# Performance work log

Measured on AMD Instinct MI355X. Metric: run time of the kernel, lower is better.

The kernel has to match this reference:

```python
import jax, jax.numpy as jnp
import numpy as np
from jax import lax

EPS = 1e-5


def setup_inputs() -> dict:
    key = jax.random.key(0)
    ks = jax.random.split(key, 8)
    b, c_in, h, w = 16, 256, 64, 64
    c_out, kh, n_exp = 512, 3, 8
    fan_in = c_in * kh * kh
    bound_w = float(np.sqrt(6.0 / fan_in))  # kaiming_uniform a=sqrt(5) -> U(-sqrt(6/fan_in), +)
    bound_b = float(1.0 / np.sqrt(fan_in))
    return {
        "x": jax.random.normal(ks[0], (b, c_in, h, w), dtype=jnp.float32),
        "expert_weight": jax.random.uniform(ks[1], (n_exp, c_out, c_in, kh, kh), jnp.float32, -bound_w, bound_w),
        "expert_bias": jax.random.uniform(ks[2], (n_exp, c_out), jnp.float32, -bound_b, bound_b),
        "fc_w": jax.random.uniform(ks[3], (n_exp, c_in), jnp.float32, -1.0 / np.sqrt(c_in), 1.0 / np.sqrt(c_in)),
        "fc_b": jax.random.uniform(ks[4], (n_exp,), jnp.float32, -1.0 / np.sqrt(c_in), 1.0 / np.sqrt(c_in)),
        "bn_gamma": jnp.ones((c_out,), jnp.float32),
        "bn_beta": jnp.zeros((c_out,), jnp.float32),
    }


def reference(x, expert_weight, expert_bias, fc_w, fc_b, bn_gamma, bn_beta):
    # --- route_func: GAP -> Linear -> sigmoid -> (b, k) ---
    pooled = x.mean(axis=(2, 3))                       # (b, c_in)
    routing = jax.nn.sigmoid(pooled @ fc_w.T + fc_b)   # (b, k)

    # --- per-sample combined kernels and biases ---
    comb_w = jnp.einsum('bk,koihw->boihw', routing, expert_weight)  # (b, c_out, c_in, kh, kw)
    comb_b = routing @ expert_bias                                  # (b, c_out)

    # --- per-sample conv (equivalent of groups=b grouped conv) ---
    def conv_one(xi, wi):
        # xi: (c_in, h, w), wi: (c_out, c_in, kh, kw)
        return lax.conv_general_dilated(
            xi[None], wi, window_strides=(1, 1), padding=[(1, 1), (1, 1)],
            rhs_dilation=(1, 1), dimension_numbers=('NCHW', 'OIHW', 'NCHW'))[0]

    out = jax.vmap(conv_one)(x, comb_w) + comb_b[:, :, None, None]  # (b, c_out, h, w)

    # --- BatchNorm2d (training mode: batch statistics) ---
    mean = out.mean(axis=(0, 2, 3))
    var = out.var(axis=(0, 2, 3))
    out = (out - mean[None, :, None, None]) * (bn_gamma * lax.rsqrt(var + EPS))[None, :, None, None] \
          + bn_beta[None, :, None, None]

    # --- LeakyReLU(0.1) ---
    return jnp.where(out > 0, out, 0.1 * out)
```

## Files before the change

### kernel.cpp

```cpp
#include <hip/hip_runtime.h>
#include <hip/hip_bf16.h>
#include <stdint.h>

typedef unsigned short u16;
typedef short bf16x8 __attribute__((ext_vector_type(8)));
typedef float f32x4 __attribute__((ext_vector_type(4)));
typedef u16 u16x8 __attribute__((ext_vector_type(8)));

#define DEVFN static __device__ __forceinline__

#define NB 16
#define CIN 256
#define HH 64
#define WW 64
#define COUT 512
#define NEXP 8
#define NPX 4096
#define KTOT 2304
#define NSTEP 72

DEVFN u16 bf16_rne(float f){
  union { float f; uint32_t u; } v; v.f = f;
  uint32_t u = v.u;
  return (u16)((u + 0x7fffu + ((u >> 16) & 1u)) >> 16);
}

DEVFN void gload16(const void* g, void* l){
  __builtin_amdgcn_global_load_lds((const __attribute__((address_space(1))) void*)g,
                                   (__attribute__((address_space(3))) void*)l,
                                   16, 0, 0);
}

__global__ void k_pool(const float* __restrict__ x, float* __restrict__ pooled){
  int bc = blockIdx.x;
  const float4* p4 = (const float4*)(x + (size_t)bc * NPX);
  int t = threadIdx.x;
  float s = 0.f;
  for (int i = t; i < NPX/4; i += 256){ float4 v = p4[i]; s += v.x+v.y+v.z+v.w; }
  for (int o = 32; o; o >>= 1) s += __shfl_down(s, o);
  __shared__ float ls[4];
  if ((t & 63) == 0) ls[t >> 6] = s;
  __syncthreads();
  if (t == 0) pooled[bc] = (ls[0]+ls[1]+ls[2]+ls[3]) * (1.0f/ (float)NPX);
}

__global__ void k_route(const float* __restrict__ pooled, const float* __restrict__ fcw,
                        const float* __restrict__ fcb, float* __restrict__ routing){
  int bk = blockIdx.x;
  int b = bk >> 3, k = bk & 7;
  int l = threadIdx.x;
  float4 pv = ((const float4*)(pooled + b*CIN))[l];
  float4 wv = ((const float4*)(fcw   + k*CIN))[l];
  float s = pv.x*wv.x + pv.y*wv.y + pv.z*wv.z + pv.w*wv.w;
  for (int o = 32; o; o >>= 1) s += __shfl_down(s, o);
  if (l == 0) routing[b*8 + k] = 1.0f / (1.0f + __expf(-(s + fcb[k])));
}

__global__ void k_cbias(const float* __restrict__ routing, const float* __restrict__ eb,
                        float* __restrict__ cbias){
  int idx = blockIdx.x*256 + threadIdx.x;
  int b = idx >> 9, co = idx & 511;
  float s = 0.f;
  for (int k = 0; k < 8; k++) s += routing[b*8+k] * eb[k*COUT + co];
  cbias[idx] = s;
}

__global__ void k_wcomb(const float* __restrict__ routing, const float* __restrict__ ew,
                        u16* __restrict__ wc){
  int blk  = blockIdx.x;
  int step = blk >> 6;
  int cog  = blk & 63;
  int cb = step / 9, rs = step - cb*9;
  int t = threadIdx.x;
  int ci = t & 31, co = cog*8 + (t >> 5);
  int cig = cb*32 + ci;
  float wv[8];
#pragma unroll
  for (int k = 0; k < 8; k++)
    wv[k] = ew[(size_t)((k*COUT + co)*CIN + cig)*9 + rs];
  for (int b = 0; b < NB; b++){
    float s = 0.f;
#pragma unroll
    for (int k = 0; k < 8; k++) s += routing[b*8+k] * wv[k];
    wc[((size_t)(b*NSTEP + step)*COUT + co)*32 + ci] = bf16_rne(s);
  }
}

__global__ void k_xprep(const float* __restrict__ x, u16* __restrict__ xt){
  int blk = blockIdx.x;
  int ctile = blk & 3;
  int h = (blk >> 2) & 63;
  int b = blk >> 8;
  __shared__ u16 S[64][66];
  int t = threadIdx.x;
  {
    int ci_l = t >> 2, w0 = (t & 3) * 16;
    const float4* src = (const float4*)(x + ((size_t)((b*CIN + ctile*64 + ci_l)*HH + h)*WW + w0));
    float4 a = src[0], bb = src[1], c = src[2], d = src[3];
    u16* row = &S[ci_l][w0];
    row[0]=bf16_rne(a.x);  row[1]=bf16_rne(a.y);  row[2]=bf16_rne(a.z);  row[3]=bf16_rne(a.w);
    row[4]=bf16_rne(bb.x); row[5]=bf16_rne(bb.y); row[6]=bf16_rne(bb.z); row[7]=bf16_rne(bb.w);
    row[8]=bf16_rne(c.x);  row[9]=bf16_rne(c.y);  row[10]=bf16_rne(c.z); row[11]=bf16_rne(c.w);
    row[12]=bf16_rne(d.x); row[13]=bf16_rne(d.y); row[14]=bf16_rne(d.z); row[15]=bf16_rne(d.w);
  }
  __syncthreads();
  {
    int w_l = t >> 2, cig = (t & 3) * 16;
    u16x8 v0, v1;
#pragma unroll
    for (int j = 0; j < 8; j++){ v0[j] = S[cig+j][w_l]; v1[j] = S[cig+8+j][w_l]; }
    u16* dst = xt + ((size_t)(b*66 + h + 1)*68 + (w_l + 1))*CIN + ctile*64 + cig;
    *(u16x8*)(dst)     = v0;
    *(u16x8*)(dst + 8) = v1;
  }
}

#define XBYTES 17408
#define WBYTES 8192

__global__ __launch_bounds__(256, 2) void k_conv(
    const u16* __restrict__ xt, const u16* __restrict__ wc,
    const float* __restrict__ cbias, float* __restrict__ out,
    float* __restrict__ ssum, float* __restrict__ ssq)
{
  __shared__ char lds[2*XBYTES + 2*WBYTES];
  char* Xb0 = lds;
  char* Xb1 = lds + XBYTES;
  char* Wb0 = lds + 2*XBYTES;
  char* Wb1 = lds + 2*XBYTES + WBYTES;

  int hw = blockIdx.x;
  int lb = (hw & 7) * 256 + (hw >> 3);
  int b  = lb >> 7;
  int ct = (lb >> 5) & 3;
  int pt = lb & 31;
  int h0 = pt * 2;

  int t = threadIdx.x, l = t & 63, wv = t >> 6;
  int wm = wv >> 1, wn = wv & 1;
  int l15 = l & 15, kbq = l >> 4;

  const u16* xtb = xt + (size_t)b * 66*68*CIN;
  const u16* wcb = wc + (size_t)(b*NSTEP) * COUT*32 + ct*128*32;


  f32x4 acc[4][4];
#pragma unroll
  for (int m = 0; m < 4; m++)
#pragma unroll
    for (int n = 0; n < 4; n++) acc[m][n] = (f32x4){0.f,0.f,0.f,0.f};

  const int byteA0 = (wm*64 + l15)*64 + ((kbq ^ ((l15 >> 1) & 3)) << 4);

  {
#pragma unroll
    for (int i = 0; i < 5; i++){
      int qb = i*256 + wv*64;
      if (qb < 1088){
        int q = qb + l;
        int t2 = q >> 2;
        int lr = (t2 * 964) >> 16;
        int c  = t2 - lr*68;
        int j  = q & 3;
        const u16* src = xtb + ((size_t)(h0 + lr)*68 + c)*CIN + 0*32 + ((j ^ ((c >> 1) & 3)) << 3);
        gload16(src, Xb0 + qb*16);
      }
    }
#pragma unroll
    for (int i = 0; i < 2; i++){
      int q = i*256 + wv*64 + l;
      int co_l = q >> 2, j = q & 3;
      const u16* src = wcb + co_l*32 + ((j ^ ((co_l >> 1) & 3)) << 3);
      gload16(src, Wb0 + (i*256 + wv*64)*16);
    }
  }
  __syncthreads();

  int step = 0;
  for (int cb = 0; cb < 8; cb++){
    char* Xc = (cb & 1) ? Xb1 : Xb0;
    char* Xn = (cb & 1) ? Xb0 : Xb1;
#pragma unroll
    for (int rs = 0; rs < 9; rs++, step++){
      const int r = rs / 3, s = rs - r*3;
      if (step < NSTEP-1){
        char* Wn = ((step+1) & 1) ? Wb1 : Wb0;
        const u16* wstep = wcb + (size_t)(step+1)*COUT*32;
#pragma unroll
        for (int i = 0; i < 2; i++){
          int q = i*256 + wv*64 + l;
          int co_l = q >> 2, j = q & 3;
          gload16(wstep + co_l*32 + ((j ^ ((co_l >> 1) & 3)) << 3),
                  Wn + (i*256 + wv*64)*16);
        }
      }
      if (rs == 8 && cb < 7){
#pragma unroll
        for (int i = 0; i < 5; i++){
          int qb = i*256 + wv*64;
          if (qb < 1088){
            int q = qb + l;
            int t2 = q >> 2;
            int lr = (t2 * 964) >> 16;
            int c  = t2 - lr*68;
            int j  = q & 3;
            const u16* src = xtb + ((size_t)(h0 + lr)*68 + c)*CIN + (cb+1)*32 + ((j ^ ((c >> 1) & 3)) << 3);
            gload16(src, Xn + qb*16);
          }
        }
      }

      char* Wc = (step & 1) ? Wb1 : Wb0;
      int c0 = l15 + s;
      int byteB0 = ((wn + r)*68 + c0)*64 + ((kbq ^ ((c0 >> 1) & 3)) << 4);

      bf16x8 af[4], bfr[4];
#pragma unroll
      for (int m = 0; m < 4; m++) af[m]  = *(const bf16x8*)(Wc + byteA0 + m*1024);
#pragma unroll
      for (int n = 0; n < 4; n++) bfr[n] = *(const bf16x8*)(Xc + byteB0 + n*1024);
#pragma unroll
      for (int m = 0; m < 4; m++)
#pragma unroll
        for (int n = 0; n < 4; n++)
          acc[m][n] = __builtin_amdgcn_mfma_f32_16x16x32_bf16(af[m], bfr[n], acc[m][n], 0, 0, 0);

      __syncthreads();
    }
  }

  int co_t = ct*128 + wm*64 + (kbq << 2);
  int px_t = pt*128 + wn*64 + l15;
  float* outb = out + (size_t)b * COUT * NPX;
#pragma unroll
  for (int m = 0; m < 4; m++){
#pragma unroll
    for (int rg = 0; rg < 4; rg++){
      int co = co_t + m*16 + rg;
      float bias = cbias[b*COUT + co];
      float s1 = 0.f, s2 = 0.f;
      size_t base = (size_t)co * NPX + px_t;
#pragma unroll
      for (int n = 0; n < 4; n++){
        float v = acc[m][n][rg] + bias;
        outb[base + n*16] = v;
        s1 += v; s2 += v*v;
      }
#pragma unroll
      for (int o = 8; o; o >>= 1){ s1 += __shfl_xor(s1, o); s2 += __shfl_xor(s2, o); }
      if (l15 == 0){ atomicAdd(&ssum[co], s1); atomicAdd(&ssq[co], s2); }
    }
  }
}

__global__ void k_stats(const float* __restrict__ ssum, const float* __restrict__ ssq,
                        const float* __restrict__ gamma, const float* __restrict__ beta,
                        float* __restrict__ sc, float* __restrict__ sh){
  int co = blockIdx.x*256 + threadIdx.x;
  const float invN = 1.0f / 65536.0f;
  float m  = ssum[co] * invN;
  float var = ssq[co] * invN - m*m;
  float scale = gamma[co] * rsqrtf(var + 1e-5f);
  sc[co] = scale;
  sh[co] = beta[co] - m*scale;
}

__global__ void k_norm(float* __restrict__ out, const float* __restrict__ sc,
                       const float* __restrict__ sh){
  const int NF4 = (NB*COUT*NPX)/4;
  int idx = blockIdx.x*256 + threadIdx.x;
  float4* o4 = (float4*)out;
  for (int i = idx; i < NF4; i += 8192*256){
    float4 v = o4[i];
    int co = (i >> 10) & 511;
    float a = sc[co], d = sh[co];
    v.x = fmaf(v.x, a, d); v.y = fmaf(v.y, a, d);
    v.z = fmaf(v.z, a, d); v.w = fmaf(v.w, a, d);
    v.x = v.x > 0.f ? v.x : 0.1f*v.x;
    v.y = v.y > 0.f ? v.y : 0.1f*v.y;
    v.z = v.z > 0.f ? v.z : 0.1f*v.z;
    v.w = v.w > 0.f ? v.w : 0.1f*v.w;
    o4[i] = v;
  }
}

extern "C" void kernel_launch(void* const* d_in, const int* in_sizes, int n_in,
                              void* d_out, int out_size, void* d_ws, size_t ws_size,
                              hipStream_t stream) {
  const float* x     = (const float*)d_in[0];
  const float* ew    = (const float*)d_in[1];
  const float* eb    = (const float*)d_in[2];
  const float* fcw   = (const float*)d_in[3];
  const float* fcb   = (const float*)d_in[4];
  const float* gamma = (const float*)d_in[5];
  const float* beta  = (const float*)d_in[6];
  float* out = (float*)d_out;

  char* ws = (char*)d_ws;
  const size_t XT_BYTES = (size_t)NB*66*68*CIN*2;
  const size_t WC_BYTES = (size_t)NB*NSTEP*COUT*32*2;
  u16* xt = (u16*)ws;
  u16* wc = (u16*)(ws + XT_BYTES);
  float* fbase   = (float*)(ws + XT_BYTES + WC_BYTES);
  float* pooled  = fbase;
  float* routing = fbase + 4096;
  float* cbias   = fbase + 4096 + 128;
  float* ssum    = cbias + 8192;
  float* ssq     = ssum + 512;
  float* sc      = ssq + 512;
  float* sh      = sc + 512;

  hipMemsetAsync(xt, 0, XT_BYTES, stream);
  hipMemsetAsync(ssum, 0, 2*512*sizeof(float), stream);

  k_pool <<<4096, 256, 0, stream>>>(x, pooled);
  k_xprep<<<4096, 256, 0, stream>>>(x, xt);
  k_route<<<128,   64, 0, stream>>>(pooled, fcw, fcb, routing);
  k_cbias<<<32,   256, 0, stream>>>(routing, eb, cbias);
  k_wcomb<<<4608, 256, 0, stream>>>(routing, ew, wc);
  k_conv <<<2048, 256, 0, stream>>>(xt, wc, cbias, out, ssum, ssq);
  k_stats<<<2,    256, 0, stream>>>(ssum, ssq, gamma, beta, sc, sh);
  k_norm <<<8192, 256, 0, stream>>>(out, sc, sh);
}
```

Measured before the change: 331.6 us.

## Triple-buffer weight tiles and issue prefetch earlier with explicit vmcnt waits

The conv main loop moves from a double-buffered weight tile to a triple buffer, so each weight tile is prefetched two steps ahead. The next input-channel X tile is now issued earlier, at step 5 instead of step 8. Manual s_waitcnt vmcnt counts plus raw s_barrier with sched_barrier replace __syncthreads, so outstanding global-to-LDS loads need not fully drain at every step. MFMA blocks are wrapped in s_setprio to favour the math waves. This raises LDS use by one weight buffer, which may affect occupancy, and depends on the hand-counted vmcnt values being correct. The X staging also issues redundant duplicate loads in place of the guarded tail.

Result: no change. 337.9 us (+1.9%).

```diff
diff --git a/kernel.cpp b/kernel.cpp
--- a/kernel.cpp
+++ b/kernel.cpp
@@ -16,7 +16,6 @@
 #define COUT 512
 #define NEXP 8
 #define NPX 4096
-#define KTOT 2304
 #define NSTEP 72
 
 DEVFN u16 bf16_rne(float f){
@@ -30,6 +29,11 @@
                                    (__attribute__((address_space(3))) void*)l,
                                    16, 0, 0);
 }
+
+#define VMWAIT(N) asm volatile("s_waitcnt vmcnt(" #N ")" ::: "memory")
+#define BARRIER() do { __builtin_amdgcn_s_barrier(); \
+                       __builtin_amdgcn_sched_barrier(0); \
+                       asm volatile("" ::: "memory"); } while(0)
 
 __global__ void k_pool(const float* __restrict__ x, float* __restrict__ pooled){
   int bc = blockIdx.x;
@@ -118,16 +122,91 @@
 #define XBYTES 17408
 #define WBYTES 8192
 
+DEVFN void stage_w(const u16* __restrict__ wstep, char* dst, int wv, int l){
+#pragma unroll
+  for (int i = 0; i < 2; i++){
+    int q = i*256 + wv*64 + l;
+    int co_l = q >> 2, j = q & 3;
+    gload16(wstep + co_l*32 + ((j ^ ((co_l >> 1) & 3)) << 3), dst + (i*256 + wv*64)*16);
+  }
+  __builtin_amdgcn_sched_barrier(0);
+}
+
+DEVFN void stage_x(const u16* __restrict__ xtb, int h0, int cioff, char* dst, int wv, int l){
+#pragma unroll
+  for (int i = 0; i < 5; i++){
+    int qb = i*256 + wv*64;
+    if (qb >= 1088) qb -= 1088;
+    int q = qb + l;
+    int t2 = q >> 2;
+    int lr = (t2 * 964) >> 16;
+    int c  = t2 - lr*68;
+    int j  = q & 3;
+    gload16(xtb + ((size_t)(h0 + lr)*68 + c)*CIN + cioff + ((j ^ ((c >> 1) & 3)) << 3),
+            dst + qb*16);
+  }
+  __builtin_amdgcn_sched_barrier(0);
+}
+
+template<int RS>
+DEVFN void conv_step(int cb, char* w0, char* w1, char* w2,
+                     const char* Xc, char* Xn,
+                     const u16* __restrict__ xtb, const u16* __restrict__ wcb, int h0,
+                     int wv, int l, int wn, int l15, int kbq, int byteA0,
+                     f32x4 acc[4][4])
+{
+  constexpr int r = RS / 3, s = RS - r*3;
+  char* Wc = (RS % 3 == 0) ? w0 : (RS % 3 == 1) ? w1 : w2;
+  char* Wp = ((RS+2) % 3 == 0) ? w0 : ((RS+2) % 3 == 1) ? w1 : w2;
+
+  int c0 = l15 + s;
+  int byteB0 = ((wn + r)*68 + c0)*64 + ((kbq ^ ((c0 >> 1) & 3)) << 4);
+  bf16x8 af[4], bfr[4];
+#pragma unroll
+  for (int m = 0; m < 4; m++) af[m]  = *(const bf16x8*)(Wc + byteA0 + m*1024);
+#pragma unroll
+  for (int n = 0; n < 4; n++) bfr[n] = *(const bf16x8*)(Xc + byteB0 + n*1024);
+
+  if constexpr (RS < 7) {
+    stage_w(wcb + (size_t)(cb*9 + RS + 2)*(COUT*32), Wp, wv, l);
+  } else {
+    if (cb != 7) stage_w(wcb + (size_t)(cb*9 + RS + 2)*(COUT*32), Wp, wv, l);
+  }
+  if constexpr (RS == 5) {
+    if (cb != 7) stage_x(xtb, h0, (cb+1)*32, Xn, wv, l);
+  }
+
+  __builtin_amdgcn_s_setprio(1);
+#pragma unroll
+  for (int m = 0; m < 4; m++)
+#pragma unroll
+    for (int n = 0; n < 4; n++)
+      acc[m][n] = __builtin_amdgcn_mfma_f32_16x16x32_bf16(af[m], bfr[n], acc[m][n], 0, 0, 0);
+  __builtin_amdgcn_s_setprio(0);
+
+  if constexpr (RS <= 4)      { VMWAIT(2); BARRIER(); }
+  else if constexpr (RS == 5 || RS == 6) {
+    if (cb != 7) { VMWAIT(7); } else { VMWAIT(2); }
+    BARRIER();
+  }
+  else if constexpr (RS == 7) {
+    if (cb != 7) { VMWAIT(2); } else { VMWAIT(0); }
+    BARRIER();
+  }
+  else                        { if (cb != 7) { VMWAIT(2); BARRIER(); } }
+}
+
 __global__ __launch_bounds__(256, 2) void k_conv(
     const u16* __restrict__ xt, const u16* __restrict__ wc,
     const float* __restrict__ cbias, float* __restrict__ out,
     float* __restrict__ ssum, float* __restrict__ ssq)
 {
-  __shared__ char lds[2*XBYTES + 2*WBYTES];
-  char* Xb0 = lds;
-  char* Xb1 = lds + XBYTES;
-  char* Wb0 = lds + 2*XBYTES;
-  char* Wb1 = lds + 2*XBYTES + WBYTES;
+  __shared__ char lds[3*WBYTES + 2*XBYTES];
+  char* w0  = lds;
+  char* w1  = lds + WBYTES;
+  char* w2  = lds + 2*WBYTES;
+  char* Xb0 = lds + 3*WBYTES;
+  char* Xb1 = lds + 3*WBYTES + XBYTES;
 
   int hw = blockIdx.x;
   int lb = (hw & 7) * 256 + (hw >> 3);
@@ -143,7 +222,6 @@
   const u16* xtb = xt + (size_t)b * 66*68*CIN;
   const u16* wcb = wc + (size_t)(b*NSTEP) * COUT*32 + ct*128*32;
 
-
   f32x4 acc[4][4];
 #pragma unroll
   for (int m = 0; m < 4; m++)
@@ -152,81 +230,24 @@
 
   const int byteA0 = (wm*64 + l15)*64 + ((kbq ^ ((l15 >> 1) & 3)) << 4);
 
-  {
-#pragma unroll
-    for (int i = 0; i < 5; i++){
-      int qb = i*256 + wv*64;
-      if (qb < 1088){
-        int q = qb + l;
-        int t2 = q >> 2;
-        int lr = (t2 * 964) >> 16;
-        int c  = t2 - lr*68;
-        int j  = q & 3;
-        const u16* src = xtb + ((size_t)(h0 + lr)*68 + c)*CIN + 0*32 + ((j ^ ((c >> 1) & 3)) << 3);
-        gload16(src, Xb0 + qb*16);
-      }
-    }
-#pragma unroll
-    for (int i = 0; i < 2; i++){
-      int q = i*256 + wv*64 + l;
-      int co_l = q >> 2, j = q & 3;
-      const u16* src = wcb + co_l*32 + ((j ^ ((co_l >> 1) & 3)) << 3);
-      gload16(src, Wb0 + (i*256 + wv*64)*16);
-    }
-  }
-  __syncthreads();
-
-  int step = 0;
+  stage_x(xtb, h0, 0, Xb0, wv, l);
+  stage_w(wcb, w0, wv, l);
+  stage_w(wcb + COUT*32, w1, wv, l);
+  VMWAIT(2);
+  BARRIER();
+
   for (int cb = 0; cb < 8; cb++){
     char* Xc = (cb & 1) ? Xb1 : Xb0;
     char* Xn = (cb & 1) ? Xb0 : Xb1;
-#pragma unroll
-    for (int rs = 0; rs < 9; rs++, step++){
-      const int r = rs / 3, s = rs - r*3;
-      if (step < NSTEP-1){
-        char* Wn = ((step+1) & 1) ? Wb1 : Wb0;
-        const u16* wstep = wcb + (size_t)(step+1)*COUT*32;
-#pragma unroll
-        for (int i = 0; i < 2; i++){
-          int q = i*256 + wv*64 + l;
-          int co_l = q >> 2, j = q & 3;
-          gload16(wstep + co_l*32 + ((j ^ ((co_l >> 1) & 3)) << 3),
-                  Wn + (i*256 + wv*64)*16);
-        }
-      }
-      if (rs == 8 && cb < 7){
-#pragma unroll
-        for (int i = 0; i < 5; i++){
-          int qb = i*256 + wv*64;
-          if (qb < 1088){
-            int q = qb + l;
-            int t2 = q >> 2;
-            int lr = (t2 * 964) >> 16;
-            int c  = t2 - lr*68;
-            int j  = q & 3;
-            const u16* src = xtb + ((size_t)(h0 + lr)*68 + c)*CIN + (cb+1)*32 + ((j ^ ((c >> 1) & 3)) << 3);
-            gload16(src, Xn + qb*16);
-          }
-        }
-      }
-
-      char* Wc = (step & 1) ? Wb1 : Wb0;
-      int c0 = l15 + s;
-      int byteB0 = ((wn + r)*68 + c0)*64 + ((kbq ^ ((c0 >> 1) & 3)) << 4);
-
-      bf16x8 af[4], bfr[4];
-#pragma unroll
-      for (int m = 0; m < 4; m++) af[m]  = *(const bf16x8*)(Wc + byteA0 + m*1024);
-#pragma unroll
-      for (int n = 0; n < 4; n++) bfr[n] = *(const bf16x8*)(Xc + byteB0 + n*1024);
-#pragma unroll
-      for (int m = 0; m < 4; m++)
-#pragma unroll
-        for (int n = 0; n < 4; n++)
-          acc[m][n] = __builtin_amdgcn_mfma_f32_16x16x32_bf16(af[m], bfr[n], acc[m][n], 0, 0, 0);
-
-      __syncthreads();
-    }
+    conv_step<0>(cb, w0,w1,w2, Xc,Xn, xtb,wcb,h0, wv,l,wn,l15,kbq,byteA0, acc);
+    conv_step<1>(cb, w0,w1,w2, Xc,Xn, xtb,wcb,h0, wv,l,wn,l15,kbq,byteA0, acc);
+    conv_step<2>(cb, w0,w1,w2, Xc,Xn, xtb,wcb,h0, wv,l,wn,l15,kbq,byteA0, acc);
+    conv_step<3>(cb, w0,w1,w2, Xc,Xn, xtb,wcb,h0, wv,l,wn,l15,kbq,byteA0, acc);
+    conv_step<4>(cb, w0,w1,w2, Xc,Xn, xtb,wcb,h0, wv,l,wn,l15,kbq,byteA0, acc);
+    conv_step<5>(cb, w0,w1,w2, Xc,Xn, xtb,wcb,h0, wv,l,wn,l15,kbq,byteA0, acc);
+    conv_step<6>(cb, w0,w1,w2, Xc,Xn, xtb,wcb,h0, wv,l,wn,l15,kbq,byteA0, acc);
+    conv_step<7>(cb, w0,w1,w2, Xc,Xn, xtb,wcb,h0, wv,l,wn,l15,kbq,byteA0, acc);
+    conv_step<8>(cb, w0,w1,w2, Xc,Xn, xtb,wcb,h0, wv,l,wn,l15,kbq,byteA0, acc);
   }
 
   int co_t = ct*128 + wm*64 + (kbq << 2);
```
